# Optimization experiments

Hardware: AMD Instinct MI355X
Metric: run time of the kernel (lower is better)

The kernel has to match this reference:

```python
import jax, jax.numpy as jnp
import numpy as np

N, R, M = 2048, 8, 4096  # samples, rank, signal length (M even)


def setup_inputs() -> dict:
    key = jax.random.key(0)
    kW, kH, kT = jax.random.split(key, 3)
    W = jax.random.normal(kW, (N, R), dtype=jnp.float32)
    H = jax.random.normal(kH, (R, M), dtype=jnp.float32)
    # tau are per-(sample, component) time shifts; modest positive values
    tau = jax.random.uniform(kT, (N, R), dtype=jnp.float32) * 5.0
    return {"W": W, "H": H, "tau": tau}


def reference(W, H, tau):
    # W: (N, R) raw weights, H: (R, M) raw sources, tau: (N, R) shifts
    M_ = H.shape[1]
    Nf = M_ // 2 + 1
    # one-sided spectrum of the (softplus-constrained) sources
    Hf = jnp.fft.fft(jax.nn.softplus(H), axis=1)[:, :Nf]            # (R, Nf) complex
    # rebuild full mirrored spectrum: [Hf, conj(flip(Hf[:, 1:Nf-1]))] -> (R, M)
    Hft = jnp.concatenate([Hf, jnp.conj(Hf[:, 1:Nf - 1][:, ::-1])], axis=1)
    f = jnp.arange(M_, dtype=H.dtype) / M_                          # (M,) normalized freqs
    # complex exponential shift operator, (N, R, M)
    omega = jnp.exp(-2j * jnp.pi * jnp.einsum('nd,m->ndm', tau, f))
    Wf = jax.nn.softplus(W)[:, :, None] * omega                     # (N, R, M)
    # reduce over rank: V[n, m] = sum_d Wf[n, d, m] * Hft[d, m]
    V = jnp.einsum('ndm,dm->nm', Wf, Hft)                           # (N, M) complex
    return V
```

## Files before the change

### kernel.cpp

```cpp
#include <hip/hip_runtime.h>
#include <math.h>

#define MLEN 4096
#define RANK 8
#define NSAMP 2048
#define VEC 8
#define NS  4

__device__ __forceinline__ float softplus_f(float x) {
    return (x > 20.0f) ? x : log1pf(expf(x));
}

__device__ __forceinline__ float2 cmulf(float2 a, float2 b) {
    return make_float2(a.x * b.x - a.y * b.y, a.x * b.y + a.y * b.x);
}

__device__ __forceinline__ float2 wave_fft64(float2 v, int l) {
#pragma unroll
    for (int h = 32; h >= 1; h >>= 1) {
        const float tx = __shfl_xor(v.x, h);
        const float ty = __shfl_xor(v.y, h);
        const bool hi = (l & h) != 0;
        const float s = hi ? -1.0f : 1.0f;
        float2 u = make_float2(fmaf(s, v.x, tx), fmaf(s, v.y, ty));
        const int idx = hi ? (l & (h - 1)) : 0;
        const float ang = -3.14159265358979323846f * (float)idx / (float)h;
        const float cw = __cosf(ang), sw = __sinf(ang);
        v = make_float2(u.x * cw - u.y * sw, u.x * sw + u.y * cw);
    }
    return v;
}

__global__ __launch_bounds__(256) void fftA_kernel(const float* __restrict__ H,
                                                   float2* __restrict__ Z) {
    const int wid = (blockIdx.x << 2) + (threadIdx.x >> 6);
    const int l   = threadIdx.x & 63;
    const int d   = wid >> 6;
    const int n2  = wid & 63;

    const float x = softplus_f(H[d * MLEN + (l << 6) + n2]);
    float2 v = wave_fft64(make_float2(x, 0.0f), l);
    const int k1 = (int)(__brev((unsigned)l) >> 26);
    const float ang = -3.14159265358979323846f / 2048.0f * (float)(n2 * k1);
    v = cmulf(v, make_float2(__cosf(ang), __sinf(ang)));
    Z[d * MLEN + (k1 << 6) + n2] = v;
}

__global__ __launch_bounds__(256) void fftB_kernel(const float2* __restrict__ Z,
                                                   float2* __restrict__ Hft) {
    const int wid = (blockIdx.x << 2) + (threadIdx.x >> 6);
    const int l   = threadIdx.x & 63;
    const int d   = wid >> 6;
    const int k1  = wid & 63;

    float2 v = Z[d * MLEN + (k1 << 6) + l];
    v = wave_fft64(v, l);
    const int k2 = (int)(__brev((unsigned)l) >> 26);
    Hft[d * MLEN + (k2 << 6) + k1] = v;
}

template <int REAL_ONLY>
__device__ __forceinline__ void accum_rank(int d,
    const float4& h0, const float4& h1, const float4& h2, const float4& h3,
    const float* s_spw, const float* s_tau, const float2* s_step,
    float thm, float (&ar)[NS][VEC], float (&ai)[NS][VEC]) {
    float cs[NS], sn[NS], dc[NS], ds[NS];
#pragma unroll
    for (int j = 0; j < NS; ++j) {
        const float t   = s_tau[j * RANK + d];
        const float spw = s_spw[j * RANK + d];
        const float a0  = thm * t;
        cs[j] = spw * __cosf(a0);
        sn[j] = spw * __sinf(a0);
        const float2 st = s_step[j * RANK + d];
        dc[j] = st.x; ds[j] = st.y;
    }
#pragma unroll
    for (int k = 0; k < VEC; ++k) {
        const float4& hq = (k < 2) ? h0 : (k < 4) ? h1 : (k < 6) ? h2 : h3;
        const float hx = (k & 1) ? hq.z : hq.x;
        const float hy = (k & 1) ? hq.w : hq.y;
#pragma unroll
        for (int j = 0; j < NS; ++j) {
            ar[j][k] += cs[j] * hx - sn[j] * hy;
            if (!REAL_ONLY) ai[j][k] += cs[j] * hy + sn[j] * hx;
            if (k < VEC - 1) {
                const float ncs = cs[j] * dc[j] - sn[j] * ds[j];
                sn[j] = cs[j] * ds[j] + sn[j] * dc[j];
                cs[j] = ncs;
            }
        }
    }
}

template <int REAL_ONLY>
__global__ __launch_bounds__(256) void mix_kernel(const float* __restrict__ W,
                                                  const float* __restrict__ tau,
                                                  const float2* __restrict__ Hft,
                                                  float* __restrict__ out) {
    const int tid = threadIdx.x;
    const int m0  = (blockIdx.x * 256 + tid) * VEC;
    const int n0  = blockIdx.y * NS;

    __shared__ float  s_spw[NS * RANK];
    __shared__ float  s_tau[NS * RANK];
    __shared__ float2 s_step[NS * RANK];
    if (tid < NS * RANK) {
        const float t = tau[n0 * RANK + tid];
        s_spw[tid] = softplus_f(W[n0 * RANK + tid]);
        s_tau[tid] = t;
        const float a1 = -1.53398078788564122971e-3f * t;
        s_step[tid] = make_float2(__cosf(a1), __sinf(a1));
    }
    __syncthreads();

    float ar[NS][VEC];
    float ai[NS][VEC];
#pragma unroll
    for (int j = 0; j < NS; ++j)
#pragma unroll
        for (int k = 0; k < VEC; ++k) { ar[j][k] = 0.0f; ai[j][k] = 0.0f; }

    const float thm = -6.28318530717958647692f * ((float)m0 * (1.0f / (float)MLEN));

    const float4* p0 = reinterpret_cast<const float4*>(Hft + m0);
    float4 hA0 = p0[0], hA1 = p0[1], hA2 = p0[2], hA3 = p0[3];

#pragma unroll 1
    for (int d = 0; d < RANK; d += 2) {
        const float4* pB = reinterpret_cast<const float4*>(Hft + (d + 1) * MLEN + m0);
        float4 hB0 = pB[0], hB1 = pB[1], hB2 = pB[2], hB3 = pB[3];
        accum_rank<REAL_ONLY>(d, hA0, hA1, hA2, hA3, s_spw, s_tau, s_step, thm, ar, ai);
        if (d + 2 < RANK) {
            const float4* pA = reinterpret_cast<const float4*>(Hft + (d + 2) * MLEN + m0);
            hA0 = pA[0]; hA1 = pA[1]; hA2 = pA[2]; hA3 = pA[3];
        }
        accum_rank<REAL_ONLY>(d + 1, hB0, hB1, hB2, hB3, s_spw, s_tau, s_step, thm, ar, ai);
    }

#pragma unroll
    for (int j = 0; j < NS; ++j) {
        if (REAL_ONLY) {
            float* po = out + (size_t)(n0 + j) * MLEN + m0;
            float4 o0 = make_float4(ar[j][0], ar[j][1], ar[j][2], ar[j][3]);
            float4 o1 = make_float4(ar[j][4], ar[j][5], ar[j][6], ar[j][7]);
            reinterpret_cast<float4*>(po)[0] = o0;
            reinterpret_cast<float4*>(po)[1] = o1;
        } else {
            float2* po = (float2*)out + (size_t)(n0 + j) * MLEN + m0;
#pragma unroll
            for (int q = 0; q < 4; ++q) {
                float4 o = make_float4(ar[j][2 * q], ai[j][2 * q],
                                       ar[j][2 * q + 1], ai[j][2 * q + 1]);
                reinterpret_cast<float4*>(po)[q] = o;
            }
        }
    }
}

extern "C" void kernel_launch(void* const* d_in, const int* in_sizes, int n_in,
                              void* d_out, int out_size, void* d_ws, size_t ws_size,
                              hipStream_t stream) {
    const float* W   = (const float*)d_in[0];
    const float* H   = (const float*)d_in[1];
    const float* tau = (const float*)d_in[2];
    float2* Z   = (float2*)d_ws;
    float2* Hft = Z + RANK * MLEN;
    float* out  = (float*)d_out;

    fftA_kernel<<<128, 256, 0, stream>>>(H, Z);
    fftB_kernel<<<128, 256, 0, stream>>>(Z, Hft);

    const long long NM = (long long)NSAMP * MLEN;
    dim3 grid(MLEN / (256 * VEC), NSAMP / NS);
    if ((long long)out_size >= 2 * NM) {
        mix_kernel<0><<<grid, 256, 0, stream>>>(W, tau, Hft, out);
    } else {
        mix_kernel<1><<<grid, 256, 0, stream>>>(W, tau, Hft, out);
    }
}
```

Measured before the change: 33.50 us.

## Fuse two-pass FFT into one LDS-staged kernel and shrink mix tile

Merges the two global-memory FFT passes into a single kernel per rank that stages the softplus input and the intermediate spectrum in shared memory. Padding and an XOR swizzle are used to limit bank conflicts. This removes one launch and the global round trip through the workspace. Separately, the mix kernel now handles 4 frequencies and 2 samples per thread instead of 8 and 4, which quadruples the grid and lowers register pressure at the cost of more per-thread setup and more reloads of Hft. The fused FFT runs on only 8 blocks, so it leaves most of the GPU idle.

New measurement: 40.22 us. 1.2x slower.

```diff
diff --git a/kernel.cpp b/kernel.cpp
--- a/kernel.cpp
+++ b/kernel.cpp
@@ -4,8 +4,8 @@
 #define MLEN 4096
 #define RANK 8
 #define NSAMP 2048
-#define VEC 8
-#define NS  4
+#define VEC 4
+#define NS  2
 
 __device__ __forceinline__ float softplus_f(float x) {
     return (x > 20.0f) ? x : log1pf(expf(x));
@@ -31,37 +31,43 @@
     return v;
 }
 
-__global__ __launch_bounds__(256) void fftA_kernel(const float* __restrict__ H,
-                                                   float2* __restrict__ Z) {
-    const int wid = (blockIdx.x << 2) + (threadIdx.x >> 6);
-    const int l   = threadIdx.x & 63;
-    const int d   = wid >> 6;
-    const int n2  = wid & 63;
+__global__ __launch_bounds__(1024) void fft_fused_kernel(const float* __restrict__ H,
+                                                         float2* __restrict__ Hft) {
+    __shared__ float  xr[4160];
+    __shared__ float2 Zl[4096];
+    const int d   = blockIdx.x;
+    const int tid = threadIdx.x;
+    const int w   = tid >> 6;
+    const int l   = tid & 63;
 
-    const float x = softplus_f(H[d * MLEN + (l << 6) + n2]);
-    float2 v = wave_fft64(make_float2(x, 0.0f), l);
-    const int k1 = (int)(__brev((unsigned)l) >> 26);
-    const float ang = -3.14159265358979323846f / 2048.0f * (float)(n2 * k1);
-    v = cmulf(v, make_float2(__cosf(ang), __sinf(ang)));
-    Z[d * MLEN + (k1 << 6) + n2] = v;
-}
+    for (int i = tid; i < MLEN; i += 1024)
+        xr[i + (i >> 6)] = softplus_f(H[d * MLEN + i]);
+    __syncthreads();
 
-__global__ __launch_bounds__(256) void fftB_kernel(const float2* __restrict__ Z,
-                                                   float2* __restrict__ Hft) {
-    const int wid = (blockIdx.x << 2) + (threadIdx.x >> 6);
-    const int l   = threadIdx.x & 63;
-    const int d   = wid >> 6;
-    const int k1  = wid & 63;
+#pragma unroll
+    for (int c = 0; c < 4; ++c) {
+        const int n2 = w + (c << 4);
+        float2 v = wave_fft64(make_float2(xr[65 * l + n2], 0.0f), l);
+        const int k1 = (int)(__brev((unsigned)l) >> 26);
+        const float ang = -3.14159265358979323846f / 2048.0f * (float)(n2 * k1);
+        v = cmulf(v, make_float2(__cosf(ang), __sinf(ang)));
+        Zl[(k1 << 6) + (n2 ^ (k1 & 31))] = v;
+    }
+    __syncthreads();
 
-    float2 v = Z[d * MLEN + (k1 << 6) + l];
-    v = wave_fft64(v, l);
-    const int k2 = (int)(__brev((unsigned)l) >> 26);
-    Hft[d * MLEN + (k2 << 6) + k1] = v;
+#pragma unroll
+    for (int c = 0; c < 4; ++c) {
+        const int k1 = w + (c << 4);
+        float2 v = Zl[(k1 << 6) + (l ^ (k1 & 31))];
+        v = wave_fft64(v, l);
+        const int k2 = (int)(__brev((unsigned)l) >> 26);
+        Hft[d * MLEN + (k2 << 6) + k1] = v;
+    }
 }
 
 template <int REAL_ONLY>
 __device__ __forceinline__ void accum_rank(int d,
-    const float4& h0, const float4& h1, const float4& h2, const float4& h3,
+    const float4& h0, const float4& h1,
     const float* s_spw, const float* s_tau, const float2* s_step,
     float thm, float (&ar)[NS][VEC], float (&ai)[NS][VEC]) {
     float cs[NS], sn[NS], dc[NS], ds[NS];
@@ -77,9 +83,8 @@
     }
 #pragma unroll
     for (int k = 0; k < VEC; ++k) {
-        const float4& hq = (k < 2) ? h0 : (k < 4) ? h1 : (k < 6) ? h2 : h3;
-        const float hx = (k & 1) ? hq.z : hq.x;
-        const float hy = (k & 1) ? hq.w : hq.y;
+        const float hx = (k < 2) ? ((k & 1) ? h0.z : h0.x) : ((k & 1) ? h1.z : h1.x);
+        const float hy = (k < 2) ? ((k & 1) ? h0.w : h0.y) : ((k & 1) ? h1.w : h1.y);
 #pragma unroll
         for (int j = 0; j < NS; ++j) {
             ar[j][k] += cs[j] * hx - sn[j] * hy;
@@ -124,36 +129,31 @@
     const float thm = -6.28318530717958647692f * ((float)m0 * (1.0f / (float)MLEN));
 
     const float4* p0 = reinterpret_cast<const float4*>(Hft + m0);
-    float4 hA0 = p0[0], hA1 = p0[1], hA2 = p0[2], hA3 = p0[3];
+    float4 hA0 = p0[0], hA1 = p0[1];
 
 #pragma unroll 1
     for (int d = 0; d < RANK; d += 2) {
         const float4* pB = reinterpret_cast<const float4*>(Hft + (d + 1) * MLEN + m0);
-        float4 hB0 = pB[0], hB1 = pB[1], hB2 = pB[2], hB3 = pB[3];
-        accum_rank<REAL_ONLY>(d, hA0, hA1, hA2, hA3, s_spw, s_tau, s_step, thm, ar, ai);
+        float4 hB0 = pB[0], hB1 = pB[1];
+        accum_rank<REAL_ONLY>(d, hA0, hA1, s_spw, s_tau, s_step, thm, ar, ai);
         if (d + 2 < RANK) {
             const float4* pA = reinterpret_cast<const float4*>(Hft + (d + 2) * MLEN + m0);
-            hA0 = pA[0]; hA1 = pA[1]; hA2 = pA[2]; hA3 = pA[3];
+            hA0 = pA[0]; hA1 = pA[1];
         }
-        accum_rank<REAL_ONLY>(d + 1, hB0, hB1, hB2, hB3, s_spw, s_tau, s_step, thm, ar, ai);
+        accum_rank<REAL_ONLY>(d + 1, hB0, hB1, s_spw, s_tau, s_step, thm, ar, ai);
     }
 
 #pragma unroll
     for (int j = 0; j < NS; ++j) {
         if (REAL_ONLY) {
-            float* po = out + (size_t)(n0 + j) * MLEN + m0;
-            float4 o0 = make_float4(ar[j][0], ar[j][1], ar[j][2], ar[j][3]);
-            float4 o1 = make_float4(ar[j][4], ar[j][5], ar[j][6], ar[j][7]);
-            reinterpret_cast<float4*>(po)[0] = o0;
-            reinterpret_cast<float4*>(po)[1] = o1;
+            float4 o = make_float4(ar[j][0], ar[j][1], ar[j][2], ar[j][3]);
+            *reinterpret_cast<float4*>(out + (size_t)(n0 + j) * MLEN + m0) = o;
         } else {
             float2* po = (float2*)out + (size_t)(n0 + j) * MLEN + m0;
-#pragma unroll
-            for (int q = 0; q < 4; ++q) {
-                float4 o = make_float4(ar[j][2 * q], ai[j][2 * q],
-                                       ar[j][2 * q + 1], ai[j][2 * q + 1]);
-                reinterpret_cast<float4*>(po)[q] = o;
-            }
+            reinterpret_cast<float4*>(po)[0] =
+                make_float4(ar[j][0], ai[j][0], ar[j][1], ai[j][1]);
+            reinterpret_cast<float4*>(po)[1] =
+                make_float4(ar[j][2], ai[j][2], ar[j][3], ai[j][3]);
         }
     }
 }
@@ -164,12 +164,10 @@
     const float* W   = (const float*)d_in[0];
     const float* H   = (const float*)d_in[1];
     const float* tau = (const float*)d_in[2];
-    float2* Z   = (float2*)d_ws;
-    float2* Hft = Z + RANK * MLEN;
+    float2* Hft = (float2*)d_ws;
     float* out  = (float*)d_out;
 
-    fftA_kernel<<<128, 256, 0, stream>>>(H, Z);
-    fftB_kernel<<<128, 256, 0, stream>>>(Z, Hft);
+    fft_fused_kernel<<<RANK, 1024, 0, stream>>>(H, Hft);
 
     const long long NM = (long long)NSAMP * MLEN;
     dim3 grid(MLEN / (256 * VEC), NSAMP / NS);
```
